# Kernel optimization log

Measured on AMD Instinct MI355X. Metric: run time of the kernel, lower is better.

The kernel has to match this reference:

```python
import jax, jax.numpy as jnp
import numpy as np

N, E, D, R = 50000, 800000, 64, 8
NEG_SLOPE = 0.2
EPS = 1e-9


def setup_inputs() -> dict:
    key = jax.random.key(0)
    k1, k2, k3, k4, k5, k6 = jax.random.split(key, 6)
    h = jax.random.normal(k1, (N, D), dtype=jnp.float32)
    W = jax.random.normal(k2, (R, D, D), dtype=jnp.float32) / np.sqrt(D)
    a = jax.random.normal(k3, (R, 2 * D), dtype=jnp.float32) * 0.1
    dropout_mask = jnp.ones((D,), dtype=jnp.float32)
    src = jax.random.randint(k4, (E,), 0, N, dtype=jnp.int32)
    dst = jax.random.randint(k5, (E,), 0, N, dtype=jnp.int32)
    etype = jax.random.randint(k6, (E,), 0, R, dtype=jnp.int32)
    return {"h": h, "W": W, "a": a, "dropout_mask": dropout_mask,
            "src": src, "dst": dst, "etype": etype}


def reference(h, W, a, dropout_mask, src, dst, etype):
    # message_func: relation-specific transform of source node states.
    # Compute h @ W_r for all relations once ([R,N,D]), then gather per edge.
    hW = jnp.einsum('nd,rde->rne', h, W)          # [R, N, D]
    msg = hW[etype, src]                           # [E, D] gather
    # attention logits: a_r . [h_dst, msg], leaky relu
    e = (jnp.sum(h[dst] * a[etype, :D], axis=-1)
         + jnp.sum(msg * a[etype, D:], axis=-1))   # [E]
    e = jnp.where(e > 0, e, NEG_SLOPE * e)
    # reduce_func: segment softmax over incoming edges per dst node
    m = jax.ops.segment_max(e, dst, num_segments=N)          # [N]
    w = jnp.exp(e - m[dst])                                   # [E]
    denom = jax.ops.segment_sum(w, dst, num_segments=N)      # [N]
    red = jax.ops.segment_sum(w[:, None] * msg, dst, num_segments=N)  # [N, D]
    red = red / (denom[:, None] + EPS)
    # apply_node_func: residual update modulated by shared dropout_mask buffer
    return h + red * dropout_mask
```

## Files before the change

### kernel.cpp

```cpp
#include <hip/hip_runtime.h>
#include <cstdint>
#include <cstddef>

#define N_NODES 50000
#define N_EDGES 800000
#define NE4 (N_EDGES / 4)
#define DIM 64
#define NREL 8
#define NBLK 782
#define NPAD (NBLK * 64)
#define NBUCK 196
#define NCHUNK 196
#define CHUNK4 1024
#define NP (NBUCK * NCHUNK)
#define NSCAN 151

typedef unsigned short u16;
typedef unsigned int u32;
typedef float f32x4 __attribute__((ext_vector_type(4)));
typedef short bf16x8 __attribute__((ext_vector_type(8)));

__device__ __forceinline__ u16 f2b(float f) {
  union { float f; u32 u; } c; c.f = f;
  u32 u = c.u;
  return (u16)((u + 0x7fffu + ((u >> 16) & 1u)) >> 16);
}
__device__ __forceinline__ float b2f(u16 v) {
  union { u32 u; float f; } c; c.u = ((u32)v) << 16;
  return c.f;
}

__global__ __launch_bounds__(256) void k_phase1(const int* __restrict__ dst,
                                                const float* __restrict__ W,
                                                const float* __restrict__ a,
                                                int* __restrict__ pcnt,
                                                u16* __restrict__ WbT,
                                                u16* __restrict__ Tb) {
  __shared__ int cnt[256];
  const int t = threadIdx.x;
  if (blockIdx.x < NCHUNK) {
    const int c = blockIdx.x;
    cnt[t] = 0;
    __syncthreads();
    const int base4 = c * CHUNK4;
    const int end4 = (base4 + CHUNK4 < NE4) ? base4 + CHUNK4 : NE4;
    for (int i = base4 + t; i < end4; i += 256) {
      int4 d4 = ((const int4*)dst)[i];
      atomicAdd(&cnt[d4.x >> 8], 1);
      atomicAdd(&cnt[d4.y >> 8], 1);
      atomicAdd(&cnt[d4.z >> 8], 1);
      atomicAdd(&cnt[d4.w >> 8], 1);
    }
    __syncthreads();
    if (t < NBUCK) pcnt[t * NCHUNK + c] = cnt[t];
  } else {
    const int r = blockIdx.x - NCHUNK;
    for (int idx = t; idx < DIM * DIM; idx += 256) {
      int d = idx >> 6, k = idx & 63;
      WbT[((size_t)r * DIM + d) * DIM + k] = f2b(W[((size_t)r * DIM + k) * DIM + d]);
    }
    if (t < DIM) {
      int d = t;
      const float* Wr = W + (size_t)r * DIM * DIM + (size_t)d * DIM;
      const float* ar = a + (size_t)r * 2 * DIM + DIM;
      float acc = 0.f;
      #pragma unroll
      for (int e = 0; e < DIM; ++e) acc += Wr[e] * ar[e];
      Tb[(8 + r) * DIM + d] = f2b(acc);
      Tb[r * DIM + d] = f2b(a[r * 2 * DIM + d]);
    }
  }
}

__global__ __launch_bounds__(256) void k_phase2(const float* __restrict__ h,
                                                const u16* __restrict__ Tb,
                                                const int* __restrict__ pcnt,
                                                u16* __restrict__ hb,
                                                float* __restrict__ tbl,
                                                int* __restrict__ gbase,
                                                int* __restrict__ bsum) {
  __shared__ int lds[256];
  const int t = threadIdx.x;
  if (blockIdx.x < NBLK) {
    const int wv = t >> 6;
    const int lane = t & 63;
    const int l15 = lane & 15;
    const int kg = lane >> 4;
    const int n = blockIdx.x * 64 + wv * 16 + l15;
    const int nn = (n < N_NODES) ? n : N_NODES - 1;
    const float4* hr = (const float4*)(h + (size_t)nn * DIM);
    const float4 a0 = hr[kg * 2], a1 = hr[kg * 2 + 1];
    const float4 a2 = hr[8 + kg * 2], a3 = hr[8 + kg * 2 + 1];
    union { bf16x8 v; u32 w[4]; } b0, b1;
    b0.w[0] = (u32)f2b(a0.x) | ((u32)f2b(a0.y) << 16);
    b0.w[1] = (u32)f2b(a0.z) | ((u32)f2b(a0.w) << 16);
    b0.w[2] = (u32)f2b(a1.x) | ((u32)f2b(a1.y) << 16);
    b0.w[3] = (u32)f2b(a1.z) | ((u32)f2b(a1.w) << 16);
    b1.w[0] = (u32)f2b(a2.x) | ((u32)f2b(a2.y) << 16);
    b1.w[1] = (u32)f2b(a2.z) | ((u32)f2b(a2.w) << 16);
    b1.w[2] = (u32)f2b(a3.x) | ((u32)f2b(a3.y) << 16);
    b1.w[3] = (u32)f2b(a3.z) | ((u32)f2b(a3.w) << 16);
    const bool ok = (n < N_NODES);
    if (ok) {
      *(bf16x8*)(hb + (size_t)n * DIM + kg * 8) = b0.v;
      *(bf16x8*)(hb + (size_t)n * DIM + 32 + kg * 8) = b1.v;
    }
    const bf16x8* trow = (const bf16x8*)(Tb + (size_t)l15 * DIM);
    f32x4 acc = {0.f, 0.f, 0.f, 0.f};
    acc = __builtin_amdgcn_mfma_f32_16x16x32_bf16(trow[kg], b0.v, acc, 0, 0, 0);
    acc = __builtin_amdgcn_mfma_f32_16x16x32_bf16(trow[4 + kg], b1.v, acc, 0, 0, 0);
    if (ok) *(f32x4*)(tbl + (size_t)n * 16 + kg * 4) = acc;
  } else {
    const int sid = blockIdx.x - NBLK;
    const int i = sid * 256 + t;
    const int v = (i < NP) ? pcnt[i] : 0;
    lds[t] = v;
    __syncthreads();
    #pragma unroll
    for (int off = 1; off < 256; off <<= 1) {
      int tv = (t >= off) ? lds[t - off] : 0;
      __syncthreads();
      lds[t] += tv;
      __syncthreads();
    }
    if (i < NP) gbase[i] = lds[t] - v;
    if (t == 255) bsum[sid] = lds[255];
  }
}

__global__ void k_scanB(const int* __restrict__ bsum, int* __restrict__ boff,
                        int* __restrict__ rowstart) {
  __shared__ int lds[256];
  int t = threadIdx.x;
  int v = (t < NSCAN) ? bsum[t] : 0;
  lds[t] = v;
  __syncthreads();
  #pragma unroll
  for (int off = 1; off < 256; off <<= 1) {
    int tv = (t >= off) ? lds[t - off] : 0;
    __syncthreads();
    lds[t] += tv;
    __syncthreads();
  }
  if (t < NSCAN) boff[t] = lds[t] - v;
  if (t == 0) rowstart[N_NODES] = N_EDGES;
}

__global__ __launch_bounds__(256) void k_phase4(const int* __restrict__ src,
                                                const int* __restrict__ dst,
                                                const int* __restrict__ et,
                                                const int* __restrict__ gbase,
                                                const int* __restrict__ boff,
                                                u32* __restrict__ tmp,
                                                const u16* __restrict__ hb,
                                                const u16* __restrict__ WbT,
                                                u16* __restrict__ hW) {
  __shared__ int cur[256];
  const int t = threadIdx.x;
  if (blockIdx.x < NCHUNK) {
    const int c = blockIdx.x;
    if (t < NBUCK) {
      const int idx = t * NCHUNK + c;
      cur[t] = gbase[idx] + boff[idx >> 8];
    }
    __syncthreads();
    const int base4 = c * CHUNK4;
    const int end4 = (base4 + CHUNK4 < NE4) ? base4 + CHUNK4 : NE4;
    for (int i = base4 + t; i < end4; i += 256) {
      int4 s4 = ((const int4*)src)[i];
      int4 d4 = ((const int4*)dst)[i];
      int4 t4 = ((const int4*)et)[i];
      int p0 = atomicAdd(&cur[d4.x >> 8], 1);
      int p1 = atomicAdd(&cur[d4.y >> 8], 1);
      int p2 = atomicAdd(&cur[d4.z >> 8], 1);
      int p3 = atomicAdd(&cur[d4.w >> 8], 1);
      tmp[p0] = (u32)s4.x | ((u32)t4.x << 16) | ((u32)(d4.x & 255) << 24);
      tmp[p1] = (u32)s4.y | ((u32)t4.y << 16) | ((u32)(d4.y & 255) << 24);
      tmp[p2] = (u32)s4.z | ((u32)t4.z << 16) | ((u32)(d4.z & 255) << 24);
      tmp[p3] = (u32)s4.w | ((u32)t4.w << 16) | ((u32)(d4.w & 255) << 24);
    }
  } else {
    const int bid = blockIdx.x - NCHUNK;
    const int wv = t >> 6;
    const int lane = t & 63;
    const int l15 = lane & 15;
    const int kg = lane >> 4;
    const int n = bid * 64 + wv * 16 + l15;
    const bf16x8* hrow = (const bf16x8*)(hb + (size_t)n * DIM);
    const bf16x8 b0 = hrow[kg];
    const bf16x8 b1 = hrow[4 + kg];
    const bool ok = (n < N_NODES);
    #pragma unroll
    for (int r = 0; r < NREL; ++r) {
      #pragma unroll
      for (int dt = 0; dt < 4; ++dt) {
        const int d = dt * 16 + l15;
        const bf16x8* wrow = (const bf16x8*)(WbT + ((size_t)r * DIM + d) * DIM);
        f32x4 acc = {0.f, 0.f, 0.f, 0.f};
        acc = __builtin_amdgcn_mfma_f32_16x16x32_bf16(wrow[kg], b0, acc, 0, 0, 0);
        acc = __builtin_amdgcn_mfma_f32_16x16x32_bf16(wrow[4 + kg], b1, acc, 0, 0, 0);
        if (ok) {
          uint2 s;
          s.x = (u32)f2b(acc[0]) | ((u32)f2b(acc[1]) << 16);
          s.y = (u32)f2b(acc[2]) | ((u32)f2b(acc[3]) << 16);
          *(uint2*)(hW + ((size_t)r * N_NODES + n) * DIM + dt * 16 + kg * 4) = s;
        }
      }
    }
  }
}

__global__ __launch_bounds__(256) void k_local(const u32* __restrict__ tmp,
                                               const int* __restrict__ gbase,
                                               const int* __restrict__ boff,
                                               int* __restrict__ rowstart,
                                               int* __restrict__ epk) {
  __shared__ int hist[256];
  __shared__ int excl[256];
  __shared__ int cur[256];
  const int b = blockIdx.x;
  const int t = threadIdx.x;
  const int i0 = b * NCHUNK;
  const int base = gbase[i0] + boff[i0 >> 8];
  const int end = (b == NBUCK - 1)
                      ? N_EDGES
                      : (gbase[i0 + NCHUNK] + boff[(i0 + NCHUNK) >> 8]);
  hist[t] = 0;
  cur[t] = 0;
  __syncthreads();
  for (int i = base + t; i < end; i += 256) atomicAdd(&hist[tmp[i] >> 24], 1);
  __syncthreads();
  int v = hist[t];
  excl[t] = v;
  __syncthreads();
  #pragma unroll
  for (int off = 1; off < 256; off <<= 1) {
    int tv = (t >= off) ? excl[t - off] : 0;
    __syncthreads();
    excl[t] += tv;
    __syncthreads();
  }
  int myexcl = excl[t] - v;
  excl[t] = myexcl;
  int n = b * 256 + t;
  if (n < N_NODES) rowstart[n] = base + myexcl;
  __syncthreads();
  for (int i = base + t; i < end; i += 256) {
    u32 p = tmp[i];
    int lo = p >> 24;
    int o = atomicAdd(&cur[lo], 1);
    epk[base + excl[lo] + o] = (int)(p & 0x7ffffu);
  }
}

__global__ void k_fused(const float* __restrict__ h, const u16* __restrict__ hW,
                        const float* __restrict__ tbl,
                        const int* __restrict__ rowstart, const int* __restrict__ epk,
                        const float* __restrict__ dmask, float* __restrict__ out) {
  const int node = blockIdx.x * 4 + (threadIdx.x >> 6);
  const int lane = threadIdx.x & 63;
  const int g = lane >> 2;
  const int l = lane & 3;
  const int s = rowstart[node];
  const int e = rowstart[node + 1];
  float acc[16];
  #pragma unroll
  for (int i = 0; i < 16; ++i) acc[i] = 0.f;
  float den = 0.f;
  for (int j = s; j < e; j += 16) {
    const int idx = j + g;
    const bool valid = idx < e;
    const int p = valid ? epk[idx] : 0;
    const int sv = p & 0xffff;
    const int rv = (p >> 16) & 7;
    float lg = tbl[(size_t)node * 16 + rv] + tbl[(size_t)sv * 16 + 8 + rv];
    lg = lg > 0.f ? lg : 0.2f * lg;
    const float w = valid ? __expf(lg) : 0.f;
    den += w;
    uint4 q0 = {0u, 0u, 0u, 0u}, q1 = {0u, 0u, 0u, 0u};
    if (valid) {
      const u16* row = hW + ((size_t)rv * N_NODES + sv) * DIM + l * 16;
      q0 = *(const uint4*)row;
      q1 = *(const uint4*)(row + 8);
    }
    const u32 qa[8] = {q0.x, q0.y, q0.z, q0.w, q1.x, q1.y, q1.z, q1.w};
    #pragma unroll
    for (int c = 0; c < 8; ++c) {
      acc[2 * c]     += w * b2f((u16)(qa[c] & 0xffff));
      acc[2 * c + 1] += w * b2f((u16)(qa[c] >> 16));
    }
  }
  #pragma unroll
  for (int m = 4; m <= 32; m <<= 1) {
    den += __shfl_xor(den, m, 64);
    #pragma unroll
    for (int i = 0; i < 16; ++i) acc[i] += __shfl_xor(acc[i], m, 64);
  }
  if (lane < 4) {
    const float inv = 1.f / (den + 1e-9f);
    #pragma unroll
    for (int c = 0; c < 4; ++c) {
      const float4 hv = *(const float4*)(h + (size_t)node * DIM + l * 16 + c * 4);
      const float4 dm = *(const float4*)(dmask + l * 16 + c * 4);
      float4 o;
      o.x = hv.x + acc[c * 4 + 0] * inv * dm.x;
      o.y = hv.y + acc[c * 4 + 1] * inv * dm.y;
      o.z = hv.z + acc[c * 4 + 2] * inv * dm.z;
      o.w = hv.w + acc[c * 4 + 3] * inv * dm.w;
      *(float4*)(out + (size_t)node * DIM + l * 16 + c * 4) = o;
    }
  }
}

extern "C" void kernel_launch(void* const* d_in, const int* in_sizes, int n_in,
                              void* d_out, int out_size, void* d_ws, size_t ws_size,
                              hipStream_t stream) {
  const float* h = (const float*)d_in[0];
  const float* W = (const float*)d_in[1];
  const float* a = (const float*)d_in[2];
  const float* dmask = (const float*)d_in[3];
  const int* src = (const int*)d_in[4];
  const int* dst = (const int*)d_in[5];
  const int* et = (const int*)d_in[6];
  float* out = (float*)d_out;

  char* ws = (char*)d_ws;
  size_t off = 0;
  auto alloc = [&](size_t bytes) {
    void* p = ws + off;
    off += (bytes + 255) & ~(size_t)255;
    return p;
  };
  u16* hWbuf = (u16*)alloc((size_t)NREL * N_NODES * DIM * 2);
  u16* hb = (u16*)alloc((size_t)NPAD * DIM * 2);
  u16* WbT = (u16*)alloc((size_t)NREL * DIM * DIM * 2);
  u16* Tb = (u16*)alloc(16 * DIM * 2);
  float* tbl = (float*)alloc((size_t)N_NODES * 16 * 4);
  int* rowstart = (int*)alloc((N_NODES + 1) * 4);
  int* pcnt = (int*)alloc(NP * 4);
  int* gbase = (int*)alloc(NP * 4);
  int* bsum = (int*)alloc(NSCAN * 4);
  int* boff = (int*)alloc(NSCAN * 4);
  u32* tmp = (u32*)alloc((size_t)N_EDGES * 4);
  int* epk = (int*)alloc((size_t)(N_EDGES + 64) * 4);
  (void)off; (void)ws_size;

  k_phase1<<<NCHUNK + NREL, 256, 0, stream>>>(dst, W, a, pcnt, WbT, Tb);
  k_phase2<<<NBLK + NSCAN, 256, 0, stream>>>(h, Tb, pcnt, hb, tbl, gbase, bsum);
  k_scanB<<<1, 256, 0, stream>>>(bsum, boff, rowstart);
  k_phase4<<<NCHUNK + NBLK, 256, 0, stream>>>(src, dst, et, gbase, boff, tmp, hb,
                                              WbT, hWbuf);
  k_local<<<NBUCK, 256, 0, stream>>>(tmp, gbase, boff, rowstart, epk);
  k_fused<<<N_NODES / 4, 256, 0, stream>>>(h, hWbuf, tbl, rowstart, epk, dmask, out);
}
```

Before: 108.0 us.

## Aggregate raw source features per relation, then apply W after reduction

Instead of precomputing h@W_r for all relations (a large bf16 hW buffer) and gathering 64-wide rows per edge, each destination node now accumulates weighted bf16 source features into per-relation LDS slots, 8x64 per node. One MFMA pass per 16-node block then applies the relation weights. The scan-of-block-sums kernel is folded redundantly into the partition and local kernels to drop a launch. This removes the 51MB hW write and its gather traffic. In exchange it adds LDS float atomics per edge, redundant scans in every block, and 1024-thread blocks with a large LDS footprint.

```diff
diff --git a/kernel.cpp b/kernel.cpp
--- a/kernel.cpp
+++ b/kernel.cpp
@@ -14,6 +14,7 @@
 #define CHUNK4 1024
 #define NP (NBUCK * NCHUNK)
 #define NSCAN 151
+#define SROW 516
 
 typedef unsigned short u16;
 typedef unsigned int u32;
@@ -128,103 +129,85 @@
   }
 }
 
-__global__ void k_scanB(const int* __restrict__ bsum, int* __restrict__ boff,
-                        int* __restrict__ rowstart) {
-  __shared__ int lds[256];
-  int t = threadIdx.x;
-  int v = (t < NSCAN) ? bsum[t] : 0;
-  lds[t] = v;
-  __syncthreads();
-  #pragma unroll
-  for (int off = 1; off < 256; off <<= 1) {
-    int tv = (t >= off) ? lds[t - off] : 0;
-    __syncthreads();
-    lds[t] += tv;
-    __syncthreads();
-  }
-  if (t < NSCAN) boff[t] = lds[t] - v;
-  if (t == 0) rowstart[N_NODES] = N_EDGES;
-}
-
-__global__ __launch_bounds__(256) void k_phase4(const int* __restrict__ src,
-                                                const int* __restrict__ dst,
-                                                const int* __restrict__ et,
-                                                const int* __restrict__ gbase,
-                                                const int* __restrict__ boff,
-                                                u32* __restrict__ tmp,
-                                                const u16* __restrict__ hb,
-                                                const u16* __restrict__ WbT,
-                                                u16* __restrict__ hW) {
+__global__ __launch_bounds__(256) void k_ppart(const int* __restrict__ src,
+                                               const int* __restrict__ dst,
+                                               const int* __restrict__ et,
+                                               const int* __restrict__ gbase,
+                                               const int* __restrict__ bsum,
+                                               u32* __restrict__ tmp) {
+  __shared__ int boffs[256];
   __shared__ int cur[256];
-  const int t = threadIdx.x;
-  if (blockIdx.x < NCHUNK) {
-    const int c = blockIdx.x;
-    if (t < NBUCK) {
-      const int idx = t * NCHUNK + c;
-      cur[t] = gbase[idx] + boff[idx >> 8];
-    }
-    __syncthreads();
-    const int base4 = c * CHUNK4;
-    const int end4 = (base4 + CHUNK4 < NE4) ? base4 + CHUNK4 : NE4;
-    for (int i = base4 + t; i < end4; i += 256) {
-      int4 s4 = ((const int4*)src)[i];
-      int4 d4 = ((const int4*)dst)[i];
-      int4 t4 = ((const int4*)et)[i];
-      int p0 = atomicAdd(&cur[d4.x >> 8], 1);
-      int p1 = atomicAdd(&cur[d4.y >> 8], 1);
-      int p2 = atomicAdd(&cur[d4.z >> 8], 1);
-      int p3 = atomicAdd(&cur[d4.w >> 8], 1);
-      tmp[p0] = (u32)s4.x | ((u32)t4.x << 16) | ((u32)(d4.x & 255) << 24);
-      tmp[p1] = (u32)s4.y | ((u32)t4.y << 16) | ((u32)(d4.y & 255) << 24);
-      tmp[p2] = (u32)s4.z | ((u32)t4.z << 16) | ((u32)(d4.z & 255) << 24);
-      tmp[p3] = (u32)s4.w | ((u32)t4.w << 16) | ((u32)(d4.w & 255) << 24);
-    }
-  } else {
-    const int bid = blockIdx.x - NCHUNK;
-    const int wv = t >> 6;
-    const int lane = t & 63;
-    const int l15 = lane & 15;
-    const int kg = lane >> 4;
-    const int n = bid * 64 + wv * 16 + l15;
-    const bf16x8* hrow = (const bf16x8*)(hb + (size_t)n * DIM);
-    const bf16x8 b0 = hrow[kg];
-    const bf16x8 b1 = hrow[4 + kg];
-    const bool ok = (n < N_NODES);
+  const int t = threadIdx.x, c = blockIdx.x;
+  {
+    int v = (t < NSCAN) ? bsum[t] : 0;
+    boffs[t] = v;
+    __syncthreads();
     #pragma unroll
-    for (int r = 0; r < NREL; ++r) {
-      #pragma unroll
-      for (int dt = 0; dt < 4; ++dt) {
-        const int d = dt * 16 + l15;
-        const bf16x8* wrow = (const bf16x8*)(WbT + ((size_t)r * DIM + d) * DIM);
-        f32x4 acc = {0.f, 0.f, 0.f, 0.f};
-        acc = __builtin_amdgcn_mfma_f32_16x16x32_bf16(wrow[kg], b0, acc, 0, 0, 0);
-        acc = __builtin_amdgcn_mfma_f32_16x16x32_bf16(wrow[4 + kg], b1, acc, 0, 0, 0);
-        if (ok) {
-          uint2 s;
-          s.x = (u32)f2b(acc[0]) | ((u32)f2b(acc[1]) << 16);
-          s.y = (u32)f2b(acc[2]) | ((u32)f2b(acc[3]) << 16);
-          *(uint2*)(hW + ((size_t)r * N_NODES + n) * DIM + dt * 16 + kg * 4) = s;
-        }
-      }
-    }
+    for (int off = 1; off < 256; off <<= 1) {
+      int tv = (t >= off) ? boffs[t - off] : 0;
+      __syncthreads();
+      boffs[t] += tv;
+      __syncthreads();
+    }
+    int ex = boffs[t] - v;
+    __syncthreads();
+    boffs[t] = ex;
+    __syncthreads();
+  }
+  if (t < NBUCK) {
+    const int idx = t * NCHUNK + c;
+    cur[t] = gbase[idx] + boffs[idx >> 8];
+  }
+  __syncthreads();
+  const int base4 = c * CHUNK4;
+  const int end4 = (base4 + CHUNK4 < NE4) ? base4 + CHUNK4 : NE4;
+  for (int i = base4 + t; i < end4; i += 256) {
+    int4 s4 = ((const int4*)src)[i];
+    int4 d4 = ((const int4*)dst)[i];
+    int4 t4 = ((const int4*)et)[i];
+    int p0 = atomicAdd(&cur[d4.x >> 8], 1);
+    int p1 = atomicAdd(&cur[d4.y >> 8], 1);
+    int p2 = atomicAdd(&cur[d4.z >> 8], 1);
+    int p3 = atomicAdd(&cur[d4.w >> 8], 1);
+    tmp[p0] = (u32)s4.x | ((u32)t4.x << 16) | ((u32)(d4.x & 255) << 24);
+    tmp[p1] = (u32)s4.y | ((u32)t4.y << 16) | ((u32)(d4.y & 255) << 24);
+    tmp[p2] = (u32)s4.z | ((u32)t4.z << 16) | ((u32)(d4.z & 255) << 24);
+    tmp[p3] = (u32)s4.w | ((u32)t4.w << 16) | ((u32)(d4.w & 255) << 24);
   }
 }
 
 __global__ __launch_bounds__(256) void k_local(const u32* __restrict__ tmp,
                                                const int* __restrict__ gbase,
-                                               const int* __restrict__ boff,
+                                               const int* __restrict__ bsum,
                                                int* __restrict__ rowstart,
                                                int* __restrict__ epk) {
+  __shared__ int boffs[256];
   __shared__ int hist[256];
   __shared__ int excl[256];
   __shared__ int cur[256];
   const int b = blockIdx.x;
   const int t = threadIdx.x;
+  {
+    int v = (t < NSCAN) ? bsum[t] : 0;
+    boffs[t] = v;
+    __syncthreads();
+    #pragma unroll
+    for (int off = 1; off < 256; off <<= 1) {
+      int tv = (t >= off) ? boffs[t - off] : 0;
+      __syncthreads();
+      boffs[t] += tv;
+      __syncthreads();
+    }
+    int ex = boffs[t] - v;
+    __syncthreads();
+    boffs[t] = ex;
+    __syncthreads();
+  }
   const int i0 = b * NCHUNK;
-  const int base = gbase[i0] + boff[i0 >> 8];
+  const int base = gbase[i0] + boffs[i0 >> 8];
   const int end = (b == NBUCK - 1)
                       ? N_EDGES
-                      : (gbase[i0 + NCHUNK] + boff[(i0 + NCHUNK) >> 8]);
+                      : (gbase[i0 + NCHUNK] + boffs[(i0 + NCHUNK) >> 8]);
   hist[t] = 0;
   cur[t] = 0;
   __syncthreads();
@@ -244,6 +227,7 @@
   excl[t] = myexcl;
   int n = b * 256 + t;
   if (n < N_NODES) rowstart[n] = base + myexcl;
+  if (b == NBUCK - 1 && t == 0) rowstart[N_NODES] = N_EDGES;
   __syncthreads();
   for (int i = base + t; i < end; i += 256) {
     u32 p = tmp[i];
@@ -253,62 +237,81 @@
   }
 }
 
-__global__ void k_fused(const float* __restrict__ h, const u16* __restrict__ hW,
-                        const float* __restrict__ tbl,
-                        const int* __restrict__ rowstart, const int* __restrict__ epk,
-                        const float* __restrict__ dmask, float* __restrict__ out) {
-  const int node = blockIdx.x * 4 + (threadIdx.x >> 6);
-  const int lane = threadIdx.x & 63;
-  const int g = lane >> 2;
-  const int l = lane & 3;
-  const int s = rowstart[node];
-  const int e = rowstart[node + 1];
-  float acc[16];
-  #pragma unroll
-  for (int i = 0; i < 16; ++i) acc[i] = 0.f;
-  float den = 0.f;
-  for (int j = s; j < e; j += 16) {
-    const int idx = j + g;
-    const bool valid = idx < e;
+__global__ __launch_bounds__(1024) void k_mega(const u16* __restrict__ hb,
+                                               const u16* __restrict__ WbT,
+                                               const float* __restrict__ tbl,
+                                               const int* __restrict__ rowstart,
+                                               const int* __restrict__ epk,
+                                               const float* __restrict__ h,
+                                               const float* __restrict__ dmask,
+                                               float* __restrict__ out) {
+  __shared__ float S[16][SROW];
+  __shared__ float denL[16];
+  const int t = threadIdx.x;
+  const int wv = t >> 6;
+  const int lane = t & 63;
+  for (int i = t; i < 16 * SROW; i += 1024) ((float*)S)[i] = 0.f;
+  if (t < 16) denL[t] = 0.f;
+  __syncthreads();
+
+  const int node = blockIdx.x * 16 + wv;
+  const int g = lane >> 4;
+  const int l = lane & 15;
+  const int s0 = rowstart[node];
+  const int e0 = rowstart[node + 1];
+  float dn = 0.f;
+  const float* tdst = tbl + (size_t)node * 16;
+  for (int j0 = s0; j0 < e0; j0 += 4) {
+    const int idx = j0 + g;
+    const bool valid = idx < e0;
     const int p = valid ? epk[idx] : 0;
     const int sv = p & 0xffff;
     const int rv = (p >> 16) & 7;
-    float lg = tbl[(size_t)node * 16 + rv] + tbl[(size_t)sv * 16 + 8 + rv];
+    float lg = tdst[rv] + tbl[(size_t)sv * 16 + 8 + rv];
     lg = lg > 0.f ? lg : 0.2f * lg;
     const float w = valid ? __expf(lg) : 0.f;
-    den += w;
-    uint4 q0 = {0u, 0u, 0u, 0u}, q1 = {0u, 0u, 0u, 0u};
-    if (valid) {
-      const u16* row = hW + ((size_t)rv * N_NODES + sv) * DIM + l * 16;
-      q0 = *(const uint4*)row;
-      q1 = *(const uint4*)(row + 8);
-    }
-    const u32 qa[8] = {q0.x, q0.y, q0.z, q0.w, q1.x, q1.y, q1.z, q1.w};
+    if (l == 0) dn += w;
+    const uint2 q = *(const uint2*)(hb + (size_t)sv * DIM + l * 4);
+    float* srow = &S[wv][rv * 64 + l * 4];
+    atomicAdd(srow + 0, w * b2f((u16)(q.x & 0xffff)));
+    atomicAdd(srow + 1, w * b2f((u16)(q.x >> 16)));
+    atomicAdd(srow + 2, w * b2f((u16)(q.y & 0xffff)));
+    atomicAdd(srow + 3, w * b2f((u16)(q.y >> 16)));
+  }
+  dn += __shfl_xor(dn, 16, 64);
+  dn += __shfl_xor(dn, 32, 64);
+  if (lane == 0) denL[wv] = dn;
+  __syncthreads();
+
+  if (wv < 4) {
+    const int dt = wv;
+    const int l15 = lane & 15;
+    const int kg = lane >> 4;
+    f32x4 acc = {0.f, 0.f, 0.f, 0.f};
     #pragma unroll
-    for (int c = 0; c < 8; ++c) {
-      acc[2 * c]     += w * b2f((u16)(qa[c] & 0xffff));
-      acc[2 * c + 1] += w * b2f((u16)(qa[c] >> 16));
-    }
-  }
-  #pragma unroll
-  for (int m = 4; m <= 32; m <<= 1) {
-    den += __shfl_xor(den, m, 64);
-    #pragma unroll
-    for (int i = 0; i < 16; ++i) acc[i] += __shfl_xor(acc[i], m, 64);
-  }
-  if (lane < 4) {
-    const float inv = 1.f / (den + 1e-9f);
-    #pragma unroll
-    for (int c = 0; c < 4; ++c) {
-      const float4 hv = *(const float4*)(h + (size_t)node * DIM + l * 16 + c * 4);
-      const float4 dm = *(const float4*)(dmask + l * 16 + c * 4);
-      float4 o;
-      o.x = hv.x + acc[c * 4 + 0] * inv * dm.x;
-      o.y = hv.y + acc[c * 4 + 1] * inv * dm.y;
-      o.z = hv.z + acc[c * 4 + 2] * inv * dm.z;
-      o.w = hv.w + acc[c * 4 + 3] * inv * dm.w;
-      *(float4*)(out + (size_t)node * DIM + l * 16 + c * 4) = o;
-    }
+    for (int win = 0; win < 16; ++win) {
+      const int r = win >> 1;
+      const int koff = (win & 1) * 32 + kg * 8;
+      const float* sp = &S[l15][win * 32 + kg * 8];
+      union { bf16x8 v; u32 w4[4]; } bf;
+      #pragma unroll
+      for (int q2 = 0; q2 < 4; ++q2)
+        bf.w4[q2] = (u32)f2b(sp[q2 * 2]) | ((u32)f2b(sp[q2 * 2 + 1]) << 16);
+      const bf16x8 af =
+          *(const bf16x8*)(WbT + ((size_t)r * DIM + dt * 16 + l15) * DIM + koff);
+      acc = __builtin_amdgcn_mfma_f32_16x16x32_bf16(af, bf.v, acc, 0, 0, 0);
+    }
+    const int n = blockIdx.x * 16 + l15;
+    const float inv = 1.f / (denL[l15] + 1e-9f);
+    const int d = dt * 16 + kg * 4;
+    const float4 hv = *(const float4*)(h + (size_t)n * DIM + d);
+    const float4 dm = *(const float4*)(dmask + d);
+    float4 o;
+    o.x = hv.x + acc[0] * inv * dm.x;
+    o.y = hv.y + acc[1] * inv * dm.y;
+    o.z = hv.z + acc[2] * inv * dm.z;
+    o.w = hv.w + acc[3] * inv * dm.w;
+    *(float4*)(out + (size_t)n * DIM + d) = o;
   }
 }
 
@@ -331,7 +334,6 @@
     off += (bytes + 255) & ~(size_t)255;
     return p;
   };
-  u16* hWbuf = (u16*)alloc((size_t)NREL * N_NODES * DIM * 2);
   u16* hb = (u16*)alloc((size_t)NPAD * DIM * 2);
   u16* WbT = (u16*)alloc((size_t)NREL * DIM * DIM * 2);
   u16* Tb = (u16*)alloc(16 * DIM * 2);
@@ -340,16 +342,14 @@
   int* pcnt = (int*)alloc(NP * 4);
   int* gbase = (int*)alloc(NP * 4);
   int* bsum = (int*)alloc(NSCAN * 4);
-  int* boff = (int*)alloc(NSCAN * 4);
   u32* tmp = (u32*)alloc((size_t)N_EDGES * 4);
   int* epk = (int*)alloc((size_t)(N_EDGES + 64) * 4);
   (void)off; (void)ws_size;
 
   k_phase1<<<NCHUNK + NREL, 256, 0, stream>>>(dst, W, a, pcnt, WbT, Tb);
   k_phase2<<<NBLK + NSCAN, 256, 0, stream>>>(h, Tb, pcnt, hb, tbl, gbase, bsum);
-  k_scanB<<<1, 256, 0, stream>>>(bsum, boff, rowstart);
-  k_phase4<<<NCHUNK + NBLK, 256, 0, stream>>>(src, dst, et, gbase, boff, tmp, hb,
-                                              WbT, hWbuf);
-  k_local<<<NBUCK, 256, 0, stream>>>(tmp, gbase, boff, rowstart, epk);
-  k_fused<<<N_NODES / 4, 256, 0, stream>>>(h, hWbuf, tbl, rowstart, epk, dmask, out);
-}
+  k_ppart<<<NCHUNK, 256, 0, stream>>>(src, dst, et, gbase, bsum, tmp);
+  k_local<<<NBUCK, 256, 0, stream>>>(tmp, gbase, bsum, rowstart, epk);
+  k_mega<<<N_NODES / 16, 1024, 0, stream>>>(hb, WbT, tbl, rowstart, epk, h, dmask,
+                                            out);
+}
```

Result: slower. 365.4 us (+238.5%).
